# Optimization experiments

Hardware: AMD Instinct MI355X
Metric: run time of the kernel (lower is better)

## Reference

```python
import jax, jax.numpy as jnp
import numpy as np

EPS = 1e-8

def _gn1(x, w, b):
    # GroupNorm(num_groups=1): normalize each sample over (C, T), per-channel affine.
    mean = jnp.mean(x, axis=(1, 2), keepdims=True)
    var = jnp.mean((x - mean) ** 2, axis=(1, 2), keepdims=True)
    xn = (x - mean) * jax.lax.rsqrt(var + EPS)
    return xn * w[None, :, None] + b[None, :, None]

def _film(h, e, gw, gb, bw, bb):
    # gamma/beta: Linear -> ReLU (dropout is identity in eval), broadcast over time.
    gamma = jax.nn.relu(e @ gw.T + gb)  # [B, C]
    beta = jax.nn.relu(e @ bw.T + bb)   # [B, C]
    return gamma[:, :, None] * h + beta[:, :, None]

def setup_inputs() -> dict:
    key = jax.random.key(0)
    ks = jax.random.split(key, 16)
    B, C, T = 16, 256, 16000
    s = lambda k, shape, scale: jax.random.normal(k, shape, dtype=jnp.float32) * scale
    return {
        "x": s(ks[0], (B, C, T), 1.0),
        "cue": s(ks[1], (B, 512), 1.0),
        "gn_a_w": jnp.ones((C,), jnp.float32), "gn_a_b": jnp.zeros((C,), jnp.float32),
        "gn_n_w": jnp.ones((C,), jnp.float32), "gn_n_b": jnp.zeros((C,), jnp.float32),
        "f1g_w": s(ks[2], (C, 512), 0.04), "f1g_b": jnp.zeros((C,), jnp.float32),
        "f1b_w": s(ks[3], (C, 512), 0.04), "f1b_b": jnp.zeros((C,), jnp.float32),
        "ln1_w": jnp.ones((C,), jnp.float32), "ln1_b": jnp.zeros((C,), jnp.float32),
        "conv1_w": s(ks[4], (128, C), 0.06),
        "cds_w": s(ks[5], (256, 512), 0.04),
        "f2g_w": s(ks[6], (128, 256), 0.06), "f2g_b": jnp.zeros((128,), jnp.float32),
        "f2b_w": s(ks[7], (128, 256), 0.06), "f2b_b": jnp.zeros((128,), jnp.float32),
        "ln2_w": jnp.ones((128,), jnp.float32), "ln2_b": jnp.zeros((128,), jnp.float32),
        "conv2_w": s(ks[8], (256, 128), 0.08),
    }

def reference(x, cue, gn_a_w, gn_a_b, gn_n_w, gn_n_b, f1g_w, f1g_b, f1b_w, f1b_b,
              ln1_w, ln1_b, conv1_w, cds_w, f2g_w, f2g_b, f2b_w, f2b_b,
              ln2_w, ln2_b, conv2_w):
    x = _gn1(x, gn_a_w, gn_a_b)                 # norm_audio (GroupNorm(1, C))
    x = _gn1(x, gn_n_w, gn_n_b)                 # norm (GroupNorm(1, C))
    x = _film(x, cue, f1g_w, f1g_b, f1b_w, f1b_b) + x  # film1 + residual
    x = _gn1(x, ln1_w, ln1_b)                   # layer_norm1
    x = jnp.einsum('bct,oc->bot', x, conv1_w)   # 1x1 Conv1d, no bias -> [B,128,T]
    cue2 = jax.nn.relu(cue @ cds_w.T)           # cue_down_sample2 -> [B,256]
    x = _film(x, cue2, f2g_w, f2g_b, f2b_w, f2b_b) + x  # film2 + residual
    x = _gn1(x, ln2_w, ln2_b)                   # layer_norm2
    x = jnp.einsum('bct,oc->bot', x, conv2_w)   # 1x1 Conv1d -> [B,256,T]
    return x
```

## Files before the change

kernel.cpp:

```cpp
#include <hip/hip_runtime.h>
#include <hip/hip_bf16.h>
#include <hip/hip_fp16.h>

#define T_LEN   16000
#define NB      16
#define NTT     250
#define NTB     125
#define EPSV    1e-8f

typedef _Float16 f16x8 __attribute__((ext_vector_type(8)));
typedef float    f32x4 __attribute__((ext_vector_type(4)));

__device__ __forceinline__ ushort f2h(float f) {
    _Float16 h = (_Float16)f;
    return *(ushort*)&h;
}
__device__ __forceinline__ float f4c(const float4& v, int i) {
    return i == 0 ? v.x : i == 1 ? v.y : i == 2 ? v.z : v.w;
}
__device__ __forceinline__ void gld16(const ushort* g, ushort* l) {
    __builtin_amdgcn_global_load_lds(
        (const __attribute__((address_space(1))) uint*)g,
        (__attribute__((address_space(3))) uint*)l, 16, 0, 0);
}
__device__ __forceinline__ float waveRed64(float v) {
    #pragma unroll
    for (int m = 1; m <= 32; m <<= 1) v += __shfl_xor(v, m, 64);
    return v;
}
__device__ __forceinline__ float4 ntload4(const float* p) {
    f32x4 v = __builtin_nontemporal_load((const f32x4*)p);
    return make_float4(v[0], v[1], v[2], v[3]);
}

__global__ __launch_bounds__(256) void kP1_split(
    const float* __restrict__ x, ushort* __restrict__ Xp,
    float* __restrict__ sp, float* __restrict__ qp)
{
    const int tt = blockIdx.x, b = blockIdx.y;
    const int t0 = tt * 64;
    const int tid = threadIdx.x;
    const int j = tid & 15, cg = tid >> 4;
    __shared__ __align__(16) ushort Hs[64][264];

    #pragma unroll
    for (int p = 0; p < 4; ++p) {
        #pragma unroll
        for (int k = 0; k < 4; ++k) {
            const int c = k*64 + p*16 + cg;
            const float4 v = ntload4(x + ((size_t)(b*256 + c))*T_LEN + t0 + j*4);
            float s4 = 0.f, q4 = 0.f;
            #pragma unroll
            for (int i = 0; i < 4; ++i) {
                const float f = f4c(v, i);
                s4 += f; q4 += f*f;
                Hs[j*4 + i][c] = f2h(f);
            }
            #pragma unroll
            for (int m = 1; m <= 8; m <<= 1) {
                s4 += __shfl_xor(s4, m, 16);
                q4 += __shfl_xor(q4, m, 16);
            }
            if (j == 0) {
                sp[((size_t)b*NTT + tt)*256 + c] = s4;
                qp[((size_t)b*NTT + tt)*256 + c] = q4;
            }
        }
    }
    __syncthreads();
    ushort* dst = Xp + ((size_t)(b*NTT + tt)*4)*4096;
    #pragma unroll
    for (int k = 0; k < 8; ++k) {
        const int d  = tid + k*256;
        const int kc = d >> 9, r = d & 511;
        const int t  = r >> 3, us = r & 7;
        const int u  = us ^ (t & 7);
        *(uint4*)(dst + (size_t)d*8) = *(const uint4*)&Hs[t][kc*64 + u*8];
    }
}

__global__ __launch_bounds__(256) void kW1(
    const float* __restrict__ cue,
    const float* __restrict__ f1g_w, const float* __restrict__ f1g_b,
    const float* __restrict__ f1b_w, const float* __restrict__ f1b_b,
    const float* __restrict__ cds_w,
    float* __restrict__ G1, float* __restrict__ B1, float* __restrict__ CUE2)
{
    const int c = blockIdx.x;
    const int lane = threadIdx.x & 63, w = threadIdx.x >> 6;
    const float4 wg0 = *(const float4*)(f1g_w + c*512 + lane*8);
    const float4 wg1 = *(const float4*)(f1g_w + c*512 + lane*8 + 4);
    const float4 wb0 = *(const float4*)(f1b_w + c*512 + lane*8);
    const float4 wb1 = *(const float4*)(f1b_w + c*512 + lane*8 + 4);
    const float4 wc0 = *(const float4*)(cds_w + c*512 + lane*8);
    const float4 wc1 = *(const float4*)(cds_w + c*512 + lane*8 + 4);
    #pragma unroll
    for (int bb = 0; bb < 4; ++bb) {
        const int b = w*4 + bb;
        const float4 u0 = *(const float4*)(cue + b*512 + lane*8);
        const float4 u1 = *(const float4*)(cue + b*512 + lane*8 + 4);
        float g = 0.f, bt = 0.f, cv = 0.f;
        #pragma unroll
        for (int i = 0; i < 4; ++i) {
            g  = fmaf(f4c(u0,i), f4c(wg0,i), g);  g  = fmaf(f4c(u1,i), f4c(wg1,i), g);
            bt = fmaf(f4c(u0,i), f4c(wb0,i), bt); bt = fmaf(f4c(u1,i), f4c(wb1,i), bt);
            cv = fmaf(f4c(u0,i), f4c(wc0,i), cv); cv = fmaf(f4c(u1,i), f4c(wc1,i), cv);
        }
        g = waveRed64(g); bt = waveRed64(bt); cv = waveRed64(cv);
        if (lane == 0) {
            G1[b*256 + c]   = fmaxf(g + f1g_b[c], 0.f) + 1.f;
            B1[b*256 + c]   = fmaxf(bt + f1b_b[c], 0.f);
            CUE2[b*256 + c] = fmaxf(cv, 0.f);
        }
    }
}

__device__ __forceinline__ float blockSum256(float v, float* red)
{
    #pragma unroll
    for (int off = 32; off; off >>= 1) v += __shfl_down(v, off, 64);
    __syncthreads();
    if ((threadIdx.x & 63) == 0) red[threadIdx.x >> 6] = v;
    __syncthreads();
    return red[0] + red[1] + red[2] + red[3];
}

__global__ __launch_bounds__(256) void kBM(
    const float* __restrict__ sp, const float* __restrict__ qp,
    const float* __restrict__ gn_a_w, const float* __restrict__ gn_a_b,
    const float* __restrict__ gn_n_w, const float* __restrict__ gn_n_b,
    const float* __restrict__ G1, const float* __restrict__ B1,
    const float* __restrict__ ln1_w, const float* __restrict__ ln1_b,
    const float* __restrict__ CUE2,
    const float* __restrict__ f2g_w, const float* __restrict__ f2g_b,
    const float* __restrict__ f2b_w, const float* __restrict__ f2b_b,
    const float* __restrict__ conv1_w,
    float* __restrict__ a4o, float* __restrict__ G2,
    float* __restrict__ E, ushort* __restrict__ Msf)
{
    const int b = blockIdx.x;
    const int c = threadIdx.x;
    __shared__ float red[4];
    __shared__ float sa4[256], sd4[256], sc2[256], sg2[16];

    float sc = 0.f, qc = 0.f;
    for (int i = 0; i < NTT; ++i) {
        sc += sp[((size_t)b*NTT + i)*256 + c];
        qc += qp[((size_t)b*NTT + i)*256 + c];
    }

    const float Ninv = 1.f / (256.f * 16000.f);
    const float Tf = 16000.f;

    float S  = blockSum256(sc, red);
    float Q  = blockSum256(qc, red);
    float mu1 = S * Ninv;
    float var1 = Q * Ninv - mu1 * mu1;
    float r1 = rsqrtf(var1 + EPSV);
    float a1 = gn_a_w[c] * r1;
    float d1 = gn_a_b[c] - mu1 * r1 * gn_a_w[c];

    float S2 = blockSum256(a1*sc + Tf*d1, red);
    float Q2 = blockSum256(a1*a1*qc + 2.f*a1*d1*sc + Tf*d1*d1, red);
    float mu2 = S2 * Ninv;
    float var2 = Q2 * Ninv - mu2 * mu2;
    float r2 = rsqrtf(var2 + EPSV);
    float wn = gn_n_w[c];
    float a2 = wn * r2 * a1;
    float d2 = wn * r2 * (d1 - mu2) + gn_n_b[c];

    const float g1 = G1[b*256 + c];
    const float b1 = B1[b*256 + c];
    float a3 = g1 * a2;
    float d3 = g1 * d2 + b1;

    float S3 = blockSum256(a3*sc + Tf*d3, red);
    float Q3 = blockSum256(a3*a3*qc + 2.f*a3*d3*sc + Tf*d3*d3, red);
    float mu3 = S3 * Ninv;
    float var3 = Q3 * Ninv - mu3 * mu3;
    float r3 = rsqrtf(var3 + EPSV);
    float w1 = ln1_w[c];
    const float a4v = w1 * r3 * a3;
    const float d4v = w1 * r3 * (d3 - mu3) + ln1_b[c];
    sa4[c] = a4v;
    sd4[c] = d4v;
    a4o[b*256 + c] = a4v;
    sc2[c] = CUE2[b*256 + c];
    __syncthreads();

    const int oi = c >> 4, l16 = c & 15;
    for (int og = 0; og < 8; ++og) {
        const int o = og*16 + oi;
        float g = 0.f, bt = 0.f, ed = 0.f;
        #pragma unroll
        for (int q = 0; q < 4; ++q) {
            const int k0 = l16*16 + q*4;
            const float4 a  = *(const float4*)(f2g_w  + o*256 + k0);
            const float4 bb = *(const float4*)(f2b_w  + o*256 + k0);
            const float4 cc = *(const float4*)(conv1_w + o*256 + k0);
            const float4 u  = *(const float4*)(&sc2[k0]);
            const float4 dd = *(const float4*)(&sd4[k0]);
            #pragma unroll
            for (int i = 0; i < 4; ++i) {
                g  = fmaf(f4c(u,i),  f4c(a,i),  g);
                bt = fmaf(f4c(u,i),  f4c(bb,i), bt);
                ed = fmaf(f4c(dd,i), f4c(cc,i), ed);
            }
        }
        #pragma unroll
        for (int m = 1; m <= 8; m <<= 1) {
            g  += __shfl_xor(g, m, 16);
            bt += __shfl_xor(bt, m, 16);
            ed += __shfl_xor(ed, m, 16);
        }
        if (l16 == 0) {
            const float G2v = fmaxf(g + f2g_b[o], 0.f) + 1.f;
            const float B2v = fmaxf(bt + f2b_b[o], 0.f);
            G2[b*128 + o] = G2v;
            E[b*128 + o]  = G2v * ed + B2v;
            sg2[oi] = G2v;
        }
        __syncthreads();
        const float av = sa4[c];
        #pragma unroll
        for (int i = 0; i < 16; ++i) {
            const int oo = og*16 + i;
            Msf[((size_t)b*128 + oo)*256 + c] = f2h(sg2[i] * conv1_w[oo*256 + c] * av);
        }
        __syncthreads();
    }
}

__global__ __launch_bounds__(256) void kC_gemm(
    const ushort* __restrict__ Xp, const ushort* __restrict__ Msf,
    const float* __restrict__ E,
    float* __restrict__ s2p, float* __restrict__ q2p)
{
    const int tb = blockIdx.x, b = blockIdx.y;
    const int tid = threadIdx.x, lane = tid & 63, w = tid >> 6;
    const int wo = w >> 1, wt = w & 1;
    const int sub = lane >> 4, li = lane & 15;
    const int o0 = wo * 64;
    __shared__ __align__(16) ushort Bs[2][8192];
    __shared__ float sSp[2][128], sQp[2][128];

    const ushort* src = Xp + ((size_t)(b*NTT + 2*tb)*4)*4096;
    const ushort* mp  = Msf + (size_t)b*128*256;

    f32x4 acc[4][4];
    #pragma unroll
    for (int i = 0; i < 4; ++i)
        #pragma unroll
        for (int jx = 0; jx < 4; ++jx) acc[i][jx] = (f32x4){0.f,0.f,0.f,0.f};

    #pragma unroll
    for (int jj = 0; jj < 4; ++jj) {
        const int m = w*4 + jj;
        const int ch = m >> 3, off = (m & 7)*512;
        gld16(src + (size_t)ch*16384 + off + lane*8, &Bs[0][ch*4096 + off]);
    }
    __syncthreads();
    for (int kc = 0; kc < 4; ++kc) {
        const int buf = kc & 1;
        if (kc < 3) {
            #pragma unroll
            for (int jj = 0; jj < 4; ++jj) {
                const int m = w*4 + jj;
                const int ch = m >> 3, off = (m & 7)*512;
                gld16(src + (size_t)ch*16384 + (kc+1)*4096 + off + lane*8,
                      &Bs[buf^1][ch*4096 + off]);
            }
        }
        f16x8 bfr[4][2];
        #pragma unroll
        for (int ft = 0; ft < 4; ++ft) {
            const int tl = ft*16 + li;
            #pragma unroll
            for (int ks = 0; ks < 2; ++ks) {
                const int u = (4*ks + sub) ^ (tl & 7);
                bfr[ft][ks] = *(const f16x8*)&Bs[buf][wt*4096 + tl*64 + u*8];
            }
        }
        #pragma unroll
        for (int ks = 0; ks < 2; ++ks) {
            #pragma unroll
            for (int fo = 0; fo < 4; ++fo) {
                const f16x8 a = *(const f16x8*)(mp + (size_t)(o0 + fo*16 + li)*256 + kc*64 + ks*32 + 8*sub);
                #pragma unroll
                for (int ft = 0; ft < 4; ++ft)
                    acc[fo][ft] = __builtin_amdgcn_mfma_f32_16x16x32_f16(a, bfr[ft][ks], acc[fo][ft], 0, 0, 0);
            }
        }
        __syncthreads();
    }

    #pragma unroll
    for (int fo = 0; fo < 4; ++fo) {
        #pragma unroll
        for (int r = 0; r < 4; ++r) {
            const int o = o0 + fo*16 + sub*4 + r;
            const float ev = E[b*128 + o];
            float sv = 0.f, qv = 0.f;
            #pragma unroll
            for (int ft = 0; ft < 4; ++ft) {
                const float z = acc[fo][ft][r] + ev;
                sv += z; qv += z*z;
            }
            #pragma unroll
            for (int m = 1; m <= 8; m <<= 1) {
                sv += __shfl_xor(sv, m, 64);
                qv += __shfl_xor(qv, m, 64);
            }
            if (li == 0) { sSp[wt][o] = sv; sQp[wt][o] = qv; }
        }
    }
    __syncthreads();
    if (tid < 128) {
        s2p[((size_t)b*NTB + tb)*128 + tid] = sSp[0][tid] + sSp[1][tid];
        q2p[((size_t)b*NTB + tb)*128 + tid] = sQp[0][tid] + sQp[1][tid];
    }
}

__global__ __launch_bounds__(256) void kD2_buildF(
    const float* __restrict__ s2p, const float* __restrict__ q2p,
    const float* __restrict__ ln2_w, const float* __restrict__ ln2_b,
    const float* __restrict__ Ev,
    const float* __restrict__ a4, const float* __restrict__ G2,
    const float* __restrict__ conv1_w, const float* __restrict__ conv2_w,
    ushort* __restrict__ Fsf, float* __restrict__ h)
{
    const int b = blockIdx.y, pg = blockIdx.x;
    const int tid = threadIdx.x;
    __shared__ float Qs[32][128];
    __shared__ float sA2[128], sAE[128];
    __shared__ float rS[2], rQ[2];

    float s = 0.f, qq = 0.f;
    if (tid < 128) {
        for (int tb = 0; tb < NTB; ++tb) {
            s  += s2p[((size_t)b*NTB + tb)*128 + tid];
            qq += q2p[((size_t)b*NTB + tb)*128 + tid];
        }
        float S = s, Q = qq;
        #pragma unroll
        for (int off = 32; off; off >>= 1) {
            S += __shfl_down(S, off, 64);
            Q += __shfl_down(Q, off, 64);
        }
        if ((tid & 63) == 0) { rS[tid >> 6] = S; rQ[tid >> 6] = Q; }
    }
    __syncthreads();
    const float N2inv = 1.f / (128.f * 16000.f);
    const float mu  = (rS[0] + rS[1]) * N2inv;
    const float var = (rQ[0] + rQ[1]) * N2inv - mu * mu;
    const float r = rsqrtf(var + EPSV);
    if (tid < 128) {
        const float a2v = ln2_w[tid] * r;
        const float d2v = ln2_b[tid] - mu * ln2_w[tid] * r;
        sA2[tid] = a2v;
        sAE[tid] = a2v * Ev[b*128 + tid] + d2v;
    }
    __syncthreads();

    #pragma unroll
    for (int k = 0; k < 16; ++k) {
        const int idx = tid + k*256;
        const int p = idx >> 7, o = idx & 127;
        Qs[p][o] = conv2_w[(pg*32 + p)*128 + o] * sA2[o] * G2[b*128 + o];
    }
    __syncthreads();
    float acc[32];
    #pragma unroll
    for (int p = 0; p < 32; ++p) acc[p] = 0.f;
    for (int o = 0; o < 128; ++o) {
        const float mv = conv1_w[o*256 + tid];
        #pragma unroll
        for (int p = 0; p < 32; ++p) acc[p] = fmaf(Qs[p][o], mv, acc[p]);
    }
    const float a = a4[b*256 + tid];
    #pragma unroll
    for (int p = 0; p < 32; ++p) {
        const size_t idx = ((size_t)b*256 + pg*32 + p)*256 + tid;
        Fsf[idx] = f2h(acc[p] * a);
    }
    if (tid < 32) {
        const int p = pg*32 + tid;
        float hv = 0.f;
        for (int o = 0; o < 128; ++o)
            hv += conv2_w[p*128 + o] * sAE[o];
        h[b*256 + p] = hv;
    }
}

__global__ __launch_bounds__(256) void kE_gemm(
    const ushort* __restrict__ Xp, const ushort* __restrict__ Fsf,
    const float* __restrict__ h, float* __restrict__ out)
{
    const int tt = blockIdx.x, b = blockIdx.y;
    const int tid = threadIdx.x, lane = tid & 63, w = tid >> 6;
    const int sub = lane >> 4, li = lane & 15;
    const int o0 = w * 64, t0 = tt * 128;
    __shared__ __align__(16) ushort Bs[2][8192];

    const ushort* fp = Fsf + (size_t)b*65536;
    const size_t cbase = ((size_t)b*NTT + 2*tt)*4;

    f32x4 acc[4][8];
    #pragma unroll
    for (int i = 0; i < 4; ++i)
        #pragma unroll
        for (int jx = 0; jx < 8; ++jx) acc[i][jx] = (f32x4){0.f,0.f,0.f,0.f};

    #pragma unroll
    for (int jj = 0; jj < 4; ++jj) {
        const int m = w*4 + jj;
        const int half = m >> 3, mm = m & 7;
        gld16(Xp + (cbase + half*4 + 0)*4096 + mm*512 + lane*8,
              &Bs[0][half*4096 + mm*512]);
    }
    __syncthreads();
    for (int kc = 0; kc < 4; ++kc) {
        const int buf = kc & 1;
        if (kc < 3) {
            #pragma unroll
            for (int jj = 0; jj < 4; ++jj) {
                const int m = w*4 + jj;
                const int half = m >> 3, mm = m & 7;
                gld16(Xp + (cbase + half*4 + (kc+1))*4096 + mm*512 + lane*8,
                      &Bs[buf^1][half*4096 + mm*512]);
            }
        }
        #pragma unroll
        for (int ks = 0; ks < 2; ++ks) {
            f16x8 bfr[8];
            #pragma unroll
            for (int ft = 0; ft < 8; ++ft) {
                const int t = ft*16 + li;
                const int half = t >> 6, tl = t & 63;
                const int u = (4*ks + sub) ^ (tl & 7);
                bfr[ft] = *(const f16x8*)&Bs[buf][half*4096 + tl*64 + u*8];
            }
            #pragma unroll
            for (int fo = 0; fo < 4; ++fo) {
                const f16x8 a = *(const f16x8*)(fp + (size_t)(o0 + fo*16 + li)*256 + kc*64 + ks*32 + 8*sub);
                #pragma unroll
                for (int ft = 0; ft < 8; ++ft)
                    acc[fo][ft] = __builtin_amdgcn_mfma_f32_16x16x32_f16(a, bfr[ft], acc[fo][ft], 0, 0, 0);
            }
        }
        __syncthreads();
    }

    float* Ts = (float*)(&Bs[0][0]) + w * (16*68);
    #pragma unroll
    for (int fo = 0; fo < 4; ++fo) {
        float hv[4];
        #pragma unroll
        for (int r = 0; r < 4; ++r)
            hv[r] = h[b*256 + o0 + fo*16 + sub*4 + r];
        #pragma unroll
        for (int ph = 0; ph < 2; ++ph) {
            #pragma unroll
            for (int f4 = 0; f4 < 4; ++f4) {
                const int ft = ph*4 + f4;
                #pragma unroll
                for (int r = 0; r < 4; ++r)
                    Ts[(sub*4 + r)*68 + f4*16 + li] = acc[fo][ft][r] + hv[r];
            }
            #pragma unroll
            for (int it = 0; it < 4; ++it) {
                const int row = it*4 + sub;
                const f32x4 v = *(const f32x4*)&Ts[row*68 + li*4];
                __builtin_nontemporal_store(v,
                    (f32x4*)(out + ((size_t)(b*256 + o0 + fo*16 + row))*T_LEN
                             + t0 + ph*64 + li*4));
            }
            asm volatile("s_waitcnt lgkmcnt(0)" ::: "memory");
        }
    }
}

extern "C" void kernel_launch(void* const* d_in, const int* in_sizes, int n_in,
                              void* d_out, int out_size, void* d_ws, size_t ws_size,
                              hipStream_t stream)
{
    const float* x       = (const float*)d_in[0];
    const float* cue     = (const float*)d_in[1];
    const float* gn_a_w  = (const float*)d_in[2];
    const float* gn_a_b  = (const float*)d_in[3];
    const float* gn_n_w  = (const float*)d_in[4];
    const float* gn_n_b  = (const float*)d_in[5];
    const float* f1g_w   = (const float*)d_in[6];
    const float* f1g_b   = (const float*)d_in[7];
    const float* f1b_w   = (const float*)d_in[8];
    const float* f1b_b   = (const float*)d_in[9];
    const float* ln1_w   = (const float*)d_in[10];
    const float* ln1_b   = (const float*)d_in[11];
    const float* conv1_w = (const float*)d_in[12];
    const float* cds_w   = (const float*)d_in[13];
    const float* f2g_w   = (const float*)d_in[14];
    const float* f2g_b   = (const float*)d_in[15];
    const float* f2b_w   = (const float*)d_in[16];
    const float* f2b_b   = (const float*)d_in[17];
    const float* ln2_w   = (const float*)d_in[18];
    const float* ln2_b   = (const float*)d_in[19];
    const float* conv2_w = (const float*)d_in[20];
    float* out = (float*)d_out;

    float* ws = (float*)d_ws;
    float*  sp   = ws;
    float*  qp   = ws + 1024000;
    float*  G1   = ws + 2048000;
    float*  B1   = ws + 2052096;
    float*  CUE2 = ws + 2056192;
    float*  G2   = ws + 2060288;
    float*  a4   = ws + 2062336;
    float*  E    = ws + 2066432;
    float*  h    = ws + 2068480;
    float*  s2p  = ws + 2072576;
    float*  q2p  = ws + 2328576;
    ushort* Msf  = (ushort*)(ws + 2584576);
    ushort* Fsf  = (ushort*)(ws + 2846720);
    ushort* Xp   = (ushort*)(ws + 3371008);

    kP1_split<<<dim3(NTT, NB), 256, 0, stream>>>(x, Xp, sp, qp);

    kW1<<<256, 256, 0, stream>>>(cue, f1g_w, f1g_b, f1b_w, f1b_b, cds_w,
                                 G1, B1, CUE2);

    kBM<<<NB, 256, 0, stream>>>(sp, qp, gn_a_w, gn_a_b, gn_n_w, gn_n_b,
                                G1, B1, ln1_w, ln1_b, CUE2,
                                f2g_w, f2g_b, f2b_w, f2b_b, conv1_w,
                                a4, G2, E, Msf);

    kC_gemm<<<dim3(NTB, NB), 256, 0, stream>>>(Xp, Msf, E, s2p, q2p);

    kD2_buildF<<<dim3(8, NB), 256, 0, stream>>>(s2p, q2p, ln2_w, ln2_b, E,
                                                a4, G2, conv1_w, conv2_w,
                                                Fsf, h);

    kE_gemm<<<dim3(NTB, NB), 256, 0, stream>>>(Xp, Fsf, h, out);
}
```

Measured before the change: 313.7 us.

## Merge cue-weight kernel into input-split kernel, retile split and final GEMM

The small cue projection kernel (kW1) is folded into the input-conversion kernel as 256 extra blocks, which removes one launch. The input-split kernel now reads each channel's row with per-thread contiguous float4 loads. It stores the fp16 values channel-major in shared memory and transposes them when packing. The final GEMM kernel moves from 128-wide to 64-wide time tiles, doubling the grid and halving the accumulators per thread, with a dedicated shared buffer for the output transpose. The trade-offs are more strided 16-bit LDS reads during packing, and B-fragment and Fsf loads that are amortized over fewer time columns.

```diff
diff --git a/kernel.cpp b/kernel.cpp
--- a/kernel.cpp
+++ b/kernel.cpp
@@ -33,38 +33,75 @@
     return make_float4(v[0], v[1], v[2], v[3]);
 }
 
-__global__ __launch_bounds__(256) void kP1_split(
+__global__ __launch_bounds__(256) void kP1F(
     const float* __restrict__ x, ushort* __restrict__ Xp,
-    float* __restrict__ sp, float* __restrict__ qp)
-{
-    const int tt = blockIdx.x, b = blockIdx.y;
+    float* __restrict__ sp, float* __restrict__ qp,
+    const float* __restrict__ cue,
+    const float* __restrict__ f1g_w, const float* __restrict__ f1g_b,
+    const float* __restrict__ f1b_w, const float* __restrict__ f1b_b,
+    const float* __restrict__ cds_w,
+    float* __restrict__ G1, float* __restrict__ B1, float* __restrict__ CUE2)
+{
+    const int bid = blockIdx.x;
+    if (bid < 256) {
+        const int c = bid;
+        const int lane = threadIdx.x & 63, w = threadIdx.x >> 6;
+        const float4 wg0 = *(const float4*)(f1g_w + c*512 + lane*8);
+        const float4 wg1 = *(const float4*)(f1g_w + c*512 + lane*8 + 4);
+        const float4 wb0 = *(const float4*)(f1b_w + c*512 + lane*8);
+        const float4 wb1 = *(const float4*)(f1b_w + c*512 + lane*8 + 4);
+        const float4 wc0 = *(const float4*)(cds_w + c*512 + lane*8);
+        const float4 wc1 = *(const float4*)(cds_w + c*512 + lane*8 + 4);
+        #pragma unroll
+        for (int bb = 0; bb < 4; ++bb) {
+            const int b = w*4 + bb;
+            const float4 u0 = *(const float4*)(cue + b*512 + lane*8);
+            const float4 u1 = *(const float4*)(cue + b*512 + lane*8 + 4);
+            float g = 0.f, bt = 0.f, cv = 0.f;
+            #pragma unroll
+            for (int i = 0; i < 4; ++i) {
+                g  = fmaf(f4c(u0,i), f4c(wg0,i), g);  g  = fmaf(f4c(u1,i), f4c(wg1,i), g);
+                bt = fmaf(f4c(u0,i), f4c(wb0,i), bt); bt = fmaf(f4c(u1,i), f4c(wb1,i), bt);
+                cv = fmaf(f4c(u0,i), f4c(wc0,i), cv); cv = fmaf(f4c(u1,i), f4c(wc1,i), cv);
+            }
+            g = waveRed64(g); bt = waveRed64(bt); cv = waveRed64(cv);
+            if (lane == 0) {
+                G1[b*256 + c]   = fmaxf(g + f1g_b[c], 0.f) + 1.f;
+                B1[b*256 + c]   = fmaxf(bt + f1b_b[c], 0.f);
+                CUE2[b*256 + c] = fmaxf(cv, 0.f);
+            }
+        }
+        return;
+    }
+
+    const int pb = bid - 256;
+    const int b = pb / NTT, tt = pb % NTT;
     const int t0 = tt * 64;
     const int tid = threadIdx.x;
-    const int j = tid & 15, cg = tid >> 4;
-    __shared__ __align__(16) ushort Hs[64][264];
-
-    #pragma unroll
-    for (int p = 0; p < 4; ++p) {
-        #pragma unroll
-        for (int k = 0; k < 4; ++k) {
-            const int c = k*64 + p*16 + cg;
-            const float4 v = ntload4(x + ((size_t)(b*256 + c))*T_LEN + t0 + j*4);
-            float s4 = 0.f, q4 = 0.f;
-            #pragma unroll
-            for (int i = 0; i < 4; ++i) {
-                const float f = f4c(v, i);
-                s4 += f; q4 += f*f;
-                Hs[j*4 + i][c] = f2h(f);
-            }
-            #pragma unroll
-            for (int m = 1; m <= 8; m <<= 1) {
-                s4 += __shfl_xor(s4, m, 16);
-                q4 += __shfl_xor(q4, m, 16);
-            }
-            if (j == 0) {
-                sp[((size_t)b*NTT + tt)*256 + c] = s4;
-                qp[((size_t)b*NTT + tt)*256 + c] = q4;
-            }
+    const int cq = tid >> 2, jq = tid & 3;
+    __shared__ __align__(16) ushort Hs[256][68];
+
+    #pragma unroll
+    for (int cc = 0; cc < 4; ++cc) {
+        const int c = cc*64 + cq;
+        float s4 = 0.f, q4 = 0.f;
+        #pragma unroll
+        for (int i = 0; i < 4; ++i) {
+            const int ts = (jq + i*4)*4;
+            const float4 v = ntload4(x + ((size_t)(b*256 + c))*T_LEN + t0 + ts);
+            s4 += v.x + v.y + v.z + v.w;
+            q4 += v.x*v.x + v.y*v.y + v.z*v.z + v.w*v.w;
+            const ushort h0 = f2h(v.x), h1 = f2h(v.y), h2 = f2h(v.z), h3 = f2h(v.w);
+            uint2 pk;
+            pk.x = (uint)h0 | ((uint)h1 << 16);
+            pk.y = (uint)h2 | ((uint)h3 << 16);
+            *(uint2*)&Hs[c][ts] = pk;
+        }
+        s4 += __shfl_xor(s4, 1, 4); s4 += __shfl_xor(s4, 2, 4);
+        q4 += __shfl_xor(q4, 1, 4); q4 += __shfl_xor(q4, 2, 4);
+        if (jq == 0) {
+            sp[((size_t)b*NTT + tt)*256 + c] = s4;
+            qp[((size_t)b*NTT + tt)*256 + c] = q4;
         }
     }
     __syncthreads();
@@ -75,43 +112,13 @@
         const int kc = d >> 9, r = d & 511;
         const int t  = r >> 3, us = r & 7;
         const int u  = us ^ (t & 7);
-        *(uint4*)(dst + (size_t)d*8) = *(const uint4*)&Hs[t][kc*64 + u*8];
-    }
-}
-
-__global__ __launch_bounds__(256) void kW1(
-    const float* __restrict__ cue,
-    const float* __restrict__ f1g_w, const float* __restrict__ f1g_b,
-    const float* __restrict__ f1b_w, const float* __restrict__ f1b_b,
-    const float* __restrict__ cds_w,
-    float* __restrict__ G1, float* __restrict__ B1, float* __restrict__ CUE2)
-{
-    const int c = blockIdx.x;
-    const int lane = threadIdx.x & 63, w = threadIdx.x >> 6;
-    const float4 wg0 = *(const float4*)(f1g_w + c*512 + lane*8);
-    const float4 wg1 = *(const float4*)(f1g_w + c*512 + lane*8 + 4);
-    const float4 wb0 = *(const float4*)(f1b_w + c*512 + lane*8);
-    const float4 wb1 = *(const float4*)(f1b_w + c*512 + lane*8 + 4);
-    const float4 wc0 = *(const float4*)(cds_w + c*512 + lane*8);
-    const float4 wc1 = *(const float4*)(cds_w + c*512 + lane*8 + 4);
-    #pragma unroll
-    for (int bb = 0; bb < 4; ++bb) {
-        const int b = w*4 + bb;
-        const float4 u0 = *(const float4*)(cue + b*512 + lane*8);
-        const float4 u1 = *(const float4*)(cue + b*512 + lane*8 + 4);
-        float g = 0.f, bt = 0.f, cv = 0.f;
-        #pragma unroll
-        for (int i = 0; i < 4; ++i) {
-            g  = fmaf(f4c(u0,i), f4c(wg0,i), g);  g  = fmaf(f4c(u1,i), f4c(wg1,i), g);
-            bt = fmaf(f4c(u0,i), f4c(wb0,i), bt); bt = fmaf(f4c(u1,i), f4c(wb1,i), bt);
-            cv = fmaf(f4c(u0,i), f4c(wc0,i), cv); cv = fmaf(f4c(u1,i), f4c(wc1,i), cv);
-        }
-        g = waveRed64(g); bt = waveRed64(bt); cv = waveRed64(cv);
-        if (lane == 0) {
-            G1[b*256 + c]   = fmaxf(g + f1g_b[c], 0.f) + 1.f;
-            B1[b*256 + c]   = fmaxf(bt + f1b_b[c], 0.f);
-            CUE2[b*256 + c] = fmaxf(cv, 0.f);
-        }
+        const int c0 = kc*64 + u*8;
+        uint4 val;
+        val.x = (uint)Hs[c0+0][t] | ((uint)Hs[c0+1][t] << 16);
+        val.y = (uint)Hs[c0+2][t] | ((uint)Hs[c0+3][t] << 16);
+        val.z = (uint)Hs[c0+4][t] | ((uint)Hs[c0+5][t] << 16);
+        val.w = (uint)Hs[c0+6][t] | ((uint)Hs[c0+7][t] << 16);
+        *(uint4*)(dst + (size_t)d*8) = val;
     }
 }
 
@@ -399,59 +406,57 @@
     const int tt = blockIdx.x, b = blockIdx.y;
     const int tid = threadIdx.x, lane = tid & 63, w = tid >> 6;
     const int sub = lane >> 4, li = lane & 15;
-    const int o0 = w * 64, t0 = tt * 128;
-    __shared__ __align__(16) ushort Bs[2][8192];
-
-    const ushort* fp = Fsf + (size_t)b*65536;
-    const size_t cbase = ((size_t)b*NTT + 2*tt)*4;
-
-    f32x4 acc[4][8];
+    const int o0 = w * 64, t0 = tt * 64;
+    __shared__ __align__(16) ushort Bs[2][4096];
+    __shared__ __align__(16) float Ts[4][16][68];
+
+    const ushort* src = Xp + ((size_t)(b*NTT + tt)*4)*4096;
+    const ushort* fp  = Fsf + (size_t)b*65536;
+
+    f32x4 acc[4][4];
     #pragma unroll
     for (int i = 0; i < 4; ++i)
         #pragma unroll
-        for (int jx = 0; jx < 8; ++jx) acc[i][jx] = (f32x4){0.f,0.f,0.f,0.f};
-
-    #pragma unroll
-    for (int jj = 0; jj < 4; ++jj) {
-        const int m = w*4 + jj;
-        const int half = m >> 3, mm = m & 7;
-        gld16(Xp + (cbase + half*4 + 0)*4096 + mm*512 + lane*8,
-              &Bs[0][half*4096 + mm*512]);
+        for (int jx = 0; jx < 4; ++jx) acc[i][jx] = (f32x4){0.f,0.f,0.f,0.f};
+
+    #pragma unroll
+    for (int jj = 0; jj < 2; ++jj) {
+        const int m = w*2 + jj;
+        gld16(src + m*512 + lane*8, &Bs[0][m*512]);
     }
     __syncthreads();
     for (int kc = 0; kc < 4; ++kc) {
         const int buf = kc & 1;
         if (kc < 3) {
             #pragma unroll
-            for (int jj = 0; jj < 4; ++jj) {
-                const int m = w*4 + jj;
-                const int half = m >> 3, mm = m & 7;
-                gld16(Xp + (cbase + half*4 + (kc+1))*4096 + mm*512 + lane*8,
-                      &Bs[buf^1][half*4096 + mm*512]);
+            for (int jj = 0; jj < 2; ++jj) {
+                const int m = w*2 + jj;
+                gld16(src + (kc+1)*4096 + m*512 + lane*8, &Bs[buf^1][m*512]);
+            }
+        }
+        f16x8 bfr[4][2];
+        #pragma unroll
+        for (int ft = 0; ft < 4; ++ft) {
+            const int t = ft*16 + li;
+            #pragma unroll
+            for (int ks = 0; ks < 2; ++ks) {
+                const int u = (4*ks + sub) ^ (t & 7);
+                bfr[ft][ks] = *(const f16x8*)&Bs[buf][t*64 + u*8];
             }
         }
         #pragma unroll
         for (int ks = 0; ks < 2; ++ks) {
-            f16x8 bfr[8];
-            #pragma unroll
-            for (int ft = 0; ft < 8; ++ft) {
-                const int t = ft*16 + li;
-                const int half = t >> 6, tl = t & 63;
-                const int u = (4*ks + sub) ^ (tl & 7);
-                bfr[ft] = *(const f16x8*)&Bs[buf][half*4096 + tl*64 + u*8];
-            }
             #pragma unroll
             for (int fo = 0; fo < 4; ++fo) {
                 const f16x8 a = *(const f16x8*)(fp + (size_t)(o0 + fo*16 + li)*256 + kc*64 + ks*32 + 8*sub);
                 #pragma unroll
-                for (int ft = 0; ft < 8; ++ft)
-                    acc[fo][ft] = __builtin_amdgcn_mfma_f32_16x16x32_f16(a, bfr[ft], acc[fo][ft], 0, 0, 0);
+                for (int ft = 0; ft < 4; ++ft)
+                    acc[fo][ft] = __builtin_amdgcn_mfma_f32_16x16x32_f16(a, bfr[ft][ks], acc[fo][ft], 0, 0, 0);
             }
         }
         __syncthreads();
     }
 
-    float* Ts = (float*)(&Bs[0][0]) + w * (16*68);
     #pragma unroll
     for (int fo = 0; fo < 4; ++fo) {
         float hv[4];
@@ -459,23 +464,16 @@
         for (int r = 0; r < 4; ++r)
             hv[r] = h[b*256 + o0 + fo*16 + sub*4 + r];
         #pragma unroll
-        for (int ph = 0; ph < 2; ++ph) {
-            #pragma unroll
-            for (int f4 = 0; f4 < 4; ++f4) {
-                const int ft = ph*4 + f4;
-                #pragma unroll
-                for (int r = 0; r < 4; ++r)
-                    Ts[(sub*4 + r)*68 + f4*16 + li] = acc[fo][ft][r] + hv[r];
-            }
-            #pragma unroll
-            for (int it = 0; it < 4; ++it) {
-                const int row = it*4 + sub;
-                const f32x4 v = *(const f32x4*)&Ts[row*68 + li*4];
-                __builtin_nontemporal_store(v,
-                    (f32x4*)(out + ((size_t)(b*256 + o0 + fo*16 + row))*T_LEN
-                             + t0 + ph*64 + li*4));
-            }
-            asm volatile("s_waitcnt lgkmcnt(0)" ::: "memory");
+        for (int ft = 0; ft < 4; ++ft)
+            #pragma unroll
+            for (int r = 0; r < 4; ++r)
+                Ts[w][sub*4 + r][ft*16 + li] = acc[fo][ft][r] + hv[r];
+        #pragma unroll
+        for (int it = 0; it < 4; ++it) {
+            const int row = it*4 + sub;
+            const f32x4 v = *(const f32x4*)&Ts[w][row][li*4];
+            __builtin_nontemporal_store(v,
+                (f32x4*)(out + ((size_t)(b*256 + o0 + fo*16 + row))*T_LEN + t0 + li*4));
         }
     }
 }
@@ -523,10 +521,8 @@
     ushort* Fsf  = (ushort*)(ws + 2846720);
     ushort* Xp   = (ushort*)(ws + 3371008);
 
-    kP1_split<<<dim3(NTT, NB), 256, 0, stream>>>(x, Xp, sp, qp);
-
-    kW1<<<256, 256, 0, stream>>>(cue, f1g_w, f1g_b, f1b_w, f1b_b, cds_w,
-                                 G1, B1, CUE2);
+    kP1F<<<256 + NTT*NB, 256, 0, stream>>>(x, Xp, sp, qp,
+        cue, f1g_w, f1g_b, f1b_w, f1b_b, cds_w, G1, B1, CUE2);
 
     kBM<<<NB, 256, 0, stream>>>(sp, qp, gn_a_w, gn_a_b, gn_n_w, gn_n_b,
                                 G1, B1, ln1_w, ln1_b, CUE2,
@@ -539,5 +535,5 @@
                                                 a4, G2, conv1_w, conv2_w,
                                                 Fsf, h);
 
-    kE_gemm<<<dim3(NTB, NB), 256, 0, stream>>>(Xp, Fsf, h, out);
-}
+    kE_gemm<<<dim3(NTT, NB), 256, 0, stream>>>(Xp, Fsf, h, out);
+}
```

New measurement: 315.2 us. Within noise of the previous version (+0.5%).
